# Kernel optimization log

Measured on AMD Instinct MI355X. Metric: run time of the kernel, lower is better.

The kernel has to match this reference:

```python
import jax, jax.numpy as jnp
import numpy as np

N = 50000        # nodes
E = 800000       # edges
G = 256          # graphs in batch
NUM_EMB = 100    # atomic number vocab
D = 64           # atom_emb_dim (node channel dim, constant across layers)
ED = 50          # edge_dim
H = 128          # hidden_dim
L = 4            # num_conv_layers
Z = 2 * D + ED   # CGConv concat dim = 178


def setup_inputs() -> dict:
    key = jax.random.key(0)
    ks = jax.random.split(key, 12)
    x = jax.random.randint(ks[0], (N,), 0, NUM_EMB)
    edge_index = jax.random.randint(ks[1], (2, E), 0, N)
    edge_attr = jax.random.normal(ks[2], (E, ED), dtype=jnp.float32)
    batch = jnp.sort(jax.random.randint(ks[3], (N,), 0, G))
    emb = jax.random.normal(ks[4], (NUM_EMB, D), dtype=jnp.float32) * 0.1
    Wf = jax.random.normal(ks[5], (L, Z, D), dtype=jnp.float32) * (Z ** -0.5)
    bf = jnp.zeros((L, D), jnp.float32)
    Ws = jax.random.normal(ks[6], (L, Z, D), dtype=jnp.float32) * (Z ** -0.5)
    bs = jnp.zeros((L, D), jnp.float32)
    W1 = jax.random.normal(ks[7], (D, H), dtype=jnp.float32) * (D ** -0.5)
    b1 = jnp.zeros((H,), jnp.float32)
    W2 = jax.random.normal(ks[8], (H, H // 2), dtype=jnp.float32) * (H ** -0.5)
    b2 = jnp.zeros((H // 2,), jnp.float32)
    Wo = jax.random.normal(ks[9], (H // 2, 1), dtype=jnp.float32) * ((H // 2) ** -0.5)
    bo = jnp.zeros((1,), jnp.float32)
    return dict(x=x, edge_index=edge_index, edge_attr=edge_attr, batch=batch,
                emb=emb, Wf=Wf, bf=bf, Ws=Ws, bs=bs,
                W1=W1, b1=b1, W2=W2, b2=b2, Wo=Wo, bo=bo)


def reference(x, edge_index, edge_attr, batch, emb, Wf, bf, Ws, bs, W1, b1, W2, b2, Wo, bo):
    src = edge_index[0]  # x_j (source / neighbor)
    dst = edge_index[1]  # x_i (target, aggregation index) -- PyG convention
    h = emb[x]           # [N, D]
    for l in range(L):
        # CGConv message: z = [x_i, x_j, e_ij]; gated message; scatter-add; residual
        z = jnp.concatenate([h[dst], h[src], edge_attr], axis=-1)   # [E, Z]
        msg = jax.nn.sigmoid(z @ Wf[l] + bf[l]) * jax.nn.softplus(z @ Ws[l] + bs[l])  # [E, D]
        agg = jax.ops.segment_sum(msg, dst, num_segments=N)          # [N, D]
        h = jax.nn.softplus(h + agg)                                 # residual + F.softplus
    # global mean pool over graphs
    counts = jax.ops.segment_sum(jnp.ones((N, 1), h.dtype), batch, num_segments=G)
    pooled = jax.ops.segment_sum(h, batch, num_segments=G) / jnp.maximum(counts, 1.0)  # [G, D]
    g = jax.nn.relu(pooled @ W1 + b1)   # dropout is identity in eval mode
    g = jax.nn.relu(g @ W2 + b2)
    return (g @ Wo + bo).reshape(-1)    # [G]
```

## Files before the change

kernel.cpp:

```cpp
#include <hip/hip_runtime.h>
#include <hip/hip_bf16.h>
#include <hip/hip_fp16.h>
#include <math.h>

#define N_NODES 50000
#define N_EDGES 800000
#define N_GRAPHS 256
#define DIM 64
#define EDIM 50
#define HDIM 128
#define NLAYER 4
#define ZDIM (2 * DIM + EDIM)
#define NTILES (N_EDGES / 32)

typedef _Float16 f16;
typedef __attribute__((ext_vector_type(4))) _Float16 half4v;
typedef __attribute__((ext_vector_type(8))) _Float16 half8v;
typedef __attribute__((ext_vector_type(16))) float f32x16;

__device__ __forceinline__ float softplus_f(float x) {
    return fmaxf(x, 0.0f) + log1pf(__expf(-fabsf(x)));
}

__device__ __forceinline__ float sigx(float x) {
    float t = __builtin_amdgcn_exp2f(-1.44269504f * x);
    return __builtin_amdgcn_rcpf(1.0f + t);
}
__device__ __forceinline__ float spx(float y) {
    float t = __builtin_amdgcn_exp2f(-1.44269504f * fabsf(y));
    return fmaxf(y, 0.0f) + 0.69314718f * __builtin_amdgcn_logf(1.0f + t);
}

__global__ void k_wcat(const float* __restrict__ Wf, const float* __restrict__ Ws,
                       f16* __restrict__ wcat) {
    int i = blockIdx.x * 256 + threadIdx.x;
    int l = i >> 13;
    int rem = i & 8191;
    int k = rem >> 7;
    int colv = rem & 127;
    int g = colv >> 6, d = colv & 63;
    float v = 0.0f;
    if (k < 50) {
        const float* W = g ? Ws : Wf;
        v = W[((size_t)l * ZDIM + 128 + k) * 64 + d];
    }
    wcat[i] = (f16)v;
}

__global__ void k_wnode(const float* __restrict__ Wf, const float* __restrict__ Ws,
                        f16* __restrict__ wnode) {
    int i = blockIdx.x * 256 + threadIdx.x;
    int l = i >> 14;
    int rem = i & 16383;
    int colv2 = rem >> 6;
    int k = rem & 63;
    int half = colv2 >> 7, g = (colv2 >> 6) & 1, d = colv2 & 63;
    const float* W = g ? Ws : Wf;
    wnode[i] = (f16)W[((size_t)l * ZDIM + half * 64 + k) * 64 + d];
}

__global__ void k_hist(const int* __restrict__ eidx, int* __restrict__ hist) {
    int e = blockIdx.x * 256 + threadIdx.x;
    atomicAdd(&hist[eidx[N_EDGES + e]], 1);
}

__global__ __launch_bounds__(256) void k_scan1(const int* __restrict__ hist,
                                               int* __restrict__ scanbuf,
                                               int* __restrict__ blocksums) {
    int tid = threadIdx.x;
    int i = blockIdx.x * 256 + tid;
    int v = (i < N_NODES) ? hist[i] : 0;
    int lane = tid & 63;
#pragma unroll
    for (int off = 1; off < 64; off <<= 1) {
        int u = __shfl_up(v, off);
        if (lane >= off) v += u;
    }
    __shared__ int wsum[4];
    if (lane == 63) wsum[tid >> 6] = v;
    __syncthreads();
    int w = tid >> 6;
    int add = 0;
#pragma unroll
    for (int k = 0; k < 3; ++k)
        if (k < w) add += wsum[k];
    v += add;
    if (i < N_NODES) scanbuf[i] = v;
    if (tid == 255) blocksums[blockIdx.x] = v;
}

__global__ __launch_bounds__(256) void k_scan2(int* __restrict__ blocksums, int nb) {
    int tid = threadIdx.x;
    int v = (tid < nb) ? blocksums[tid] : 0;
    int lane = tid & 63;
#pragma unroll
    for (int off = 1; off < 64; off <<= 1) {
        int u = __shfl_up(v, off);
        if (lane >= off) v += u;
    }
    __shared__ int wsum[4];
    if (lane == 63) wsum[tid >> 6] = v;
    __syncthreads();
    int w = tid >> 6;
    int add = 0;
#pragma unroll
    for (int k = 0; k < 3; ++k)
        if (k < w) add += wsum[k];
    v += add;
    if (tid < nb) blocksums[tid] = v;
}

__global__ void k_scan3(const int* __restrict__ scanbuf, const int* __restrict__ hist,
                        const int* __restrict__ blocksums, int* __restrict__ cursor) {
    int i = blockIdx.x * 256 + threadIdx.x;
    if (i >= N_NODES) return;
    int b = blockIdx.x;
    int off = b ? blocksums[b - 1] : 0;
    cursor[i] = scanbuf[i] - hist[i] + off;
}

__global__ void k_scatter(const int* __restrict__ eidx, int* __restrict__ cursor,
                          int* __restrict__ perm, int* __restrict__ permSrc,
                          int* __restrict__ permDst) {
    int e = blockIdx.x * 256 + threadIdx.x;
    int d = eidx[N_EDGES + e];
    int pos = atomicAdd(&cursor[d], 1);
    perm[pos] = e;
    permDst[pos] = d;
    permSrc[pos] = eidx[e];
}

__global__ __launch_bounds__(256) void k_eprep2(const float* __restrict__ eattr,
                                                const int* __restrict__ perm,
                                                f16* __restrict__ eattrP) {
    int i = blockIdx.x * 256 + threadIdx.x;
    int lane = i & 63;
    int tile = i >> 6;
    int pos = tile * 32 + (lane & 31);
    int h2 = lane >> 5;
    int edge = perm[pos];
    const float* erow = eattr + (size_t)edge * EDIM;
    int k0 = 8 * h2;
    float2 v[12];
#pragma unroll
    for (int kk = 0; kk < 3; ++kk) {
#pragma unroll
        for (int p = 0; p < 4; ++p) {
            v[kk * 4 + p] = *(const float2*)(erow + k0 + 16 * kk + 2 * p);
        }
    }
    float2 t48 = make_float2(0.0f, 0.0f);
    if (h2 == 0) t48 = *(const float2*)(erow + 48);

    unsigned fb = ((unsigned)tile * 4u) * 64u + (unsigned)lane;
#pragma unroll
    for (int kk = 0; kk < 3; ++kk) {
        half8v o;
#pragma unroll
        for (int p = 0; p < 4; ++p) {
            o[2 * p] = (f16)v[kk * 4 + p].x;
            o[2 * p + 1] = (f16)v[kk * 4 + p].y;
        }
        *(half8v*)&eattrP[(fb + (unsigned)kk * 64u) * 8u] = o;
    }
    half8v o;
#pragma unroll
    for (int e = 0; e < 8; ++e) o[e] = (f16)0.0f;
    o[0] = (f16)t48.x;
    o[1] = (f16)t48.y;
    *(half8v*)&eattrP[(fb + 192u) * 8u] = o;
}

template <int MODE>
__global__ __launch_bounds__(256) void k_nodemm(
    const float* __restrict__ hin, float* __restrict__ hout, float* __restrict__ agg,
    const int* __restrict__ x, const float* __restrict__ emb,
    const float* __restrict__ bf, const float* __restrict__ bs,
    const f16* __restrict__ wnode_l,
    __half* __restrict__ dstpack, __half* __restrict__ srcpack) {
    __shared__ f16 hsf[64 * 68];
    int tid = threadIdx.x;
    int w = tid >> 6, lane = tid & 63;
    int c = lane & 31, h2 = lane >> 5;
    int n0 = blockIdx.x * 64;
    for (int idx = tid; idx < 64 * 64; idx += 256) {
        int i = idx >> 6, k = idx & 63;
        int n = n0 + i;
        float v = 0.0f;
        if (n < N_NODES) {
            if (MODE == 1) {
                v = softplus_f(hin[(size_t)n * DIM + k] + agg[(size_t)n * DIM + k]);
                agg[(size_t)n * DIM + k] = 0.0f;
                hout[(size_t)n * DIM + k] = v;
            } else {
                v = emb[x[n] * DIM + k];
                hout[(size_t)n * DIM + k] = v;
            }
        }
        hsf[i * 68 + k] = (f16)v;
    }
    __syncthreads();

    half8v bfr[2][4];
#pragma unroll
    for (int nt = 0; nt < 2; ++nt) {
#pragma unroll
        for (int kk = 0; kk < 4; ++kk) {
            bfr[nt][kk] = *(const half8v*)(wnode_l + ((64 * w + 32 * nt + c) * 64 + kk * 16 + 8 * h2));
        }
    }
    float bias[2];
#pragma unroll
    for (int nt = 0; nt < 2; ++nt) {
        int d = 32 * nt + c;
        bias[nt] = (w == 0) ? bf[d] : (w == 1) ? bs[d] : 0.0f;
    }

    f32x16 acc[2][2];
#pragma unroll
    for (int mt = 0; mt < 2; ++mt)
#pragma unroll
        for (int nt = 0; nt < 2; ++nt)
#pragma unroll
            for (int i = 0; i < 16; ++i) acc[mt][nt][i] = 0.0f;

#pragma unroll
    for (int mt = 0; mt < 2; ++mt) {
        half8v afr[4];
#pragma unroll
        for (int kk = 0; kk < 4; ++kk) {
            const f16* ap = &hsf[(32 * mt + c) * 68 + kk * 16 + 8 * h2];
            half8v a;
            *(half4v*)&a = *(const half4v*)ap;
            *((half4v*)&a + 1) = *(const half4v*)(ap + 4);
            afr[kk] = a;
        }
#pragma unroll
        for (int nt = 0; nt < 2; ++nt)
#pragma unroll
            for (int kk = 0; kk < 4; ++kk)
                acc[mt][nt] = __builtin_amdgcn_mfma_f32_32x32x16_f16(afr[kk], bfr[nt][kk],
                                                                     acc[mt][nt], 0, 0, 0);
    }

    __half* outp = (w < 2) ? dstpack : srcpack;
    int colbase = (w & 1) * 64;
#pragma unroll
    for (int mt = 0; mt < 2; ++mt) {
#pragma unroll
        for (int nt = 0; nt < 2; ++nt) {
#pragma unroll
            for (int r = 0; r < 16; ++r) {
                int row = 32 * mt + (r & 3) + 8 * (r >> 2) + 4 * h2;
                int n = n0 + row;
                if (n < N_NODES) {
                    outp[(size_t)n * 128 + colbase + 32 * nt + c] =
                        __float2half(acc[mt][nt][r] + bias[nt]);
                }
            }
        }
    }
}

__global__ __launch_bounds__(256) void k_edge_s(
    const int* __restrict__ permSrc, const int* __restrict__ permDst,
    const f16* __restrict__ eattrP, const __half* __restrict__ dstpack,
    const __half* __restrict__ srcpack, const f16* __restrict__ wcat_l,
    float* __restrict__ agg) {
    __shared__ float msgV[2][64][34];
    __shared__ int dsh[32];
    int tid = threadIdx.x;
    int w = tid >> 6;
    int lane = tid & 63;
    int c = lane & 31;
    int h2 = lane >> 5;
    int col = w * 32 + c;

    half8v wfr[4];
#pragma unroll
    for (int kk = 0; kk < 4; ++kk) {
#pragma unroll
        for (int e = 0; e < 8; ++e) {
            wfr[kk][e] = wcat_l[(kk * 16 + 8 * h2 + e) * 128 + col];
        }
    }

    for (int tile = blockIdx.x; tile < NTILES; tile += gridDim.x) {
        int e0 = tile * 32;
        int tI = permDst[e0 + c];
        int sI = permSrc[e0 + c];
        if (tid < 32) dsh[tid] = tI;

        half8v efr[4];
        unsigned fb = ((unsigned)tile * 4u) * 64u + (unsigned)lane;
#pragma unroll
        for (int kk = 0; kk < 4; ++kk) {
            efr[kk] = *(const half8v*)&eattrP[(fb + (unsigned)kk * 64u) * 8u];
        }

        f32x16 acc;
#pragma unroll
        for (int i = 0; i < 16; ++i) acc[i] = 0.0f;
#pragma unroll
        for (int kk = 0; kk < 4; ++kk) {
            acc = __builtin_amdgcn_mfma_f32_32x32x16_f16(wfr[kk], efr[kk], acc, 0, 0, 0);
        }

        const __half* drow = dstpack + (((size_t)(unsigned)tI) << 7) + w * 32 + 4 * h2;
        const __half* srow = srcpack + (((size_t)(unsigned)sI) << 7) + w * 32 + 4 * h2;
        float dv[4][4], sv[4][4];
#pragma unroll
        for (int q = 0; q < 4; ++q) {
            const __half2* dp = (const __half2*)(drow + 8 * q);
            float2 lo = __half22float2(dp[0]);
            float2 hi = __half22float2(dp[1]);
            dv[q][0] = lo.x; dv[q][1] = lo.y; dv[q][2] = hi.x; dv[q][3] = hi.y;
        }
#pragma unroll
        for (int q = 0; q < 4; ++q) {
            const __half2* sp = (const __half2*)(srow + 8 * q);
            float2 lo = __half22float2(sp[0]);
            float2 hi = __half22float2(sp[1]);
            sv[q][0] = lo.x; sv[q][1] = lo.y; sv[q][2] = hi.x; sv[q][3] = hi.y;
        }

        int dbase = (w & 1) * 32 + 4 * h2;
        if (w < 2) {
#pragma unroll
            for (int q = 0; q < 4; ++q) {
#pragma unroll
                for (int i = 0; i < 4; ++i) {
                    float pre = acc[4 * q + i] + dv[q][i] + sv[q][i];
                    msgV[0][dbase + 8 * q + i][c] = sigx(pre);
                }
            }
        } else {
#pragma unroll
            for (int q = 0; q < 4; ++q) {
#pragma unroll
                for (int i = 0; i < 4; ++i) {
                    float pre = acc[4 * q + i] + dv[q][i] + sv[q][i];
                    msgV[1][dbase + 8 * q + i][c] = spx(pre);
                }
            }
        }

        __syncthreads();

        {
            int d = tid & 63;
            int base = (tid >> 6) * 8;
            float m[8];
#pragma unroll
            for (int j2 = 0; j2 < 4; ++j2) {
                float2 a = *(const float2*)&msgV[0][d][base + 2 * j2];
                float2 b = *(const float2*)&msgV[1][d][base + 2 * j2];
                m[2 * j2] = a.x * b.x;
                m[2 * j2 + 1] = a.y * b.y;
            }
            float accum = 0.0f;
            int cur = dsh[base];
#pragma unroll
            for (int j = 0; j < 8; ++j) {
                int dn = dsh[base + j];
                if (dn != cur) {
                    unsafeAtomicAdd(&agg[(unsigned)((cur << 6) + d)], accum);
                    accum = 0.0f;
                    cur = dn;
                }
                accum += m[j];
            }
            unsafeAtomicAdd(&agg[(unsigned)((cur << 6) + d)], accum);
        }
        __syncthreads();
    }
}

__global__ __launch_bounds__(256) void k_edge_u(
    const int* __restrict__ eidx, const float* __restrict__ eattr,
    const __half* __restrict__ dstpack, const __half* __restrict__ srcpack,
    const f16* __restrict__ wcat_l, float* __restrict__ agg) {
    __shared__ float msgV[2][32][64];
    __shared__ int dsh[32], ssh[32];
    int tid = threadIdx.x;
    int w = tid >> 6;
    int lane = tid & 63;
    int c = lane & 31;
    int h2 = lane >> 5;
    int col = w * 32 + c;
    int dcol = (w & 1) * 32 + c;

    half8v bfr[4];
#pragma unroll
    for (int kk = 0; kk < 4; ++kk) {
#pragma unroll
        for (int e = 0; e < 8; ++e) bfr[kk][e] = wcat_l[(kk * 16 + 8 * h2 + e) * 128 + col];
    }

    for (int tile = blockIdx.x; tile < NTILES; tile += gridDim.x) {
        int e0 = tile * 32;
        if (lane < 32) {
            dsh[lane] = eidx[N_EDGES + e0 + lane];
            ssh[lane] = eidx[e0 + lane];
        }
        half8v afr[4];
        const float* erow = eattr + (size_t)(e0 + c) * EDIM;
#pragma unroll
        for (int kk = 0; kk < 3; ++kk) {
            int k0 = kk * 16 + 8 * h2;
#pragma unroll
            for (int p = 0; p < 4; ++p) {
                float2 v = *(const float2*)(erow + k0 + 2 * p);
                afr[kk][2 * p] = (f16)v.x;
                afr[kk][2 * p + 1] = (f16)v.y;
            }
        }
        {
            half8v a;
#pragma unroll
            for (int e = 0; e < 8; ++e) a[e] = (f16)0.0f;
            if (h2 == 0) {
                float2 v = *(const float2*)(erow + 48);
                a[0] = (f16)v.x;
                a[1] = (f16)v.y;
            }
            afr[3] = a;
        }
        f32x16 acc;
#pragma unroll
        for (int i = 0; i < 16; ++i) acc[i] = 0.0f;
#pragma unroll
        for (int kk = 0; kk < 4; ++kk)
            acc = __builtin_amdgcn_mfma_f32_32x32x16_f16(afr[kk], bfr[kk], acc, 0, 0, 0);

        __builtin_amdgcn_wave_barrier();

#pragma unroll
        for (int grp = 0; grp < 2; ++grp) {
            int tI[8], sI[8];
            float dv[8], sv[8];
#pragma unroll
            for (int r = 0; r < 8; ++r) {
                int rr = grp * 8 + r;
                int row = (rr & 3) + 8 * (rr >> 2) + 4 * h2;
                tI[r] = dsh[row];
                sI[r] = ssh[row];
            }
#pragma unroll
            for (int r = 0; r < 8; ++r) {
                dv[r] = __half2float(dstpack[(unsigned)((tI[r] << 7) + col)]);
                sv[r] = __half2float(srcpack[(unsigned)((sI[r] << 7) + col)]);
            }
            float pre[8];
#pragma unroll
            for (int r = 0; r < 8; ++r) pre[r] = acc[grp * 8 + r] + dv[r] + sv[r];
            if (w < 2) {
#pragma unroll
                for (int r = 0; r < 8; ++r) {
                    int rr = grp * 8 + r;
                    int row = (rr & 3) + 8 * (rr >> 2) + 4 * h2;
                    msgV[0][row][dcol] = sigx(pre[r]);
                }
            } else {
#pragma unroll
                for (int r = 0; r < 8; ++r) {
                    int rr = grp * 8 + r;
                    int row = (rr & 3) + 8 * (rr >> 2) + 4 * h2;
                    msgV[1][row][dcol] = spx(pre[r]);
                }
            }
        }
        __syncthreads();
        {
            int d = tid & 63;
            int base = (tid >> 6) * 8;
#pragma unroll
            for (int j = 0; j < 8; ++j) {
                int row = base + j;
                float m = msgV[0][row][d] * msgV[1][row][d];
                unsafeAtomicAdd(&agg[(unsigned)((dsh[row] << 6) + d)], m);
            }
        }
        __syncthreads();
    }
}

__global__ __launch_bounds__(256) void k_pool_s(
    const float* __restrict__ h, const float* __restrict__ agg,
    const int* __restrict__ batch,
    float* __restrict__ pooled, float* __restrict__ counts) {
    int tid = threadIdx.x;
    int d = tid & 63;
    int strm = tid >> 6;
    int base = blockIdx.x * 256 + strm * 64;
    if (base >= N_NODES) return;
    int end = min(base + 64, N_NODES);
    float accum = 0.0f;
    int cnt = 0;
    int cur = batch[base];
    for (int n = base; n < end; ++n) {
        int g = batch[n];
        if (g != cur) {
            unsafeAtomicAdd(&pooled[cur * DIM + d], accum);
            if (d == 0) unsafeAtomicAdd(&counts[cur], (float)cnt);
            accum = 0.0f;
            cnt = 0;
            cur = g;
        }
        accum += softplus_f(h[(size_t)n * DIM + d] + agg[(size_t)n * DIM + d]);
        cnt++;
    }
    unsafeAtomicAdd(&pooled[cur * DIM + d], accum);
    if (d == 0) unsafeAtomicAdd(&counts[cur], (float)cnt);
}

__global__ __launch_bounds__(64) void k_mlp(
    const float* __restrict__ pooled, const float* __restrict__ counts,
    const float* __restrict__ W1, const float* __restrict__ b1,
    const float* __restrict__ W2, const float* __restrict__ b2,
    const float* __restrict__ Wo, const float* __restrict__ bo,
    float* __restrict__ out) {
    __shared__ float ps[64];
    __shared__ float h1[128];
    int g = blockIdx.x, lane = threadIdx.x;
    float cnt = fmaxf(counts[g], 1.0f);
    ps[lane] = pooled[g * DIM + lane] / cnt;
    __syncthreads();
#pragma unroll
    for (int rep = 0; rep < 2; ++rep) {
        int j = lane + rep * 64;
        float acc = b1[j];
        for (int k = 0; k < 64; ++k) acc += ps[k] * W1[k * HDIM + j];
        h1[j] = fmaxf(acc, 0.0f);
    }
    __syncthreads();
    float acc = b2[lane];
    for (int k = 0; k < 128; ++k) acc += h1[k] * W2[k * 64 + lane];
    float v = fmaxf(acc, 0.0f) * Wo[lane];
#pragma unroll
    for (int off = 32; off; off >>= 1) v += __shfl_down(v, off);
    if (lane == 0) out[g] = v + bo[0];
}

extern "C" void kernel_launch(void* const* d_in, const int* in_sizes, int n_in,
                              void* d_out, int out_size, void* d_ws, size_t ws_size,
                              hipStream_t stream) {
    const int* x = (const int*)d_in[0];
    const int* eidx = (const int*)d_in[1];
    const float* eattr = (const float*)d_in[2];
    const int* batch = (const int*)d_in[3];
    const float* emb = (const float*)d_in[4];
    const float* Wf = (const float*)d_in[5];
    const float* bf = (const float*)d_in[6];
    const float* Ws = (const float*)d_in[7];
    const float* bs = (const float*)d_in[8];
    const float* W1 = (const float*)d_in[9];
    const float* b1 = (const float*)d_in[10];
    const float* W2 = (const float*)d_in[11];
    const float* b2 = (const float*)d_in[12];
    const float* Wo = (const float*)d_in[13];
    const float* bo = (const float*)d_in[14];
    float* out = (float*)d_out;

    char* p = (char*)d_ws;
    float* h = (float*)p;        p += (size_t)N_NODES * DIM * 4;
    __half* dstpack = (__half*)p; p += (size_t)N_NODES * 2 * DIM * 2;
    __half* srcpack = (__half*)p; p += (size_t)N_NODES * 2 * DIM * 2;
    float* agg = (float*)p;      p += (size_t)N_NODES * DIM * 4;
    float* pooled = (float*)p;   p += (size_t)N_GRAPHS * DIM * 4;
    float* counts = (float*)p;   p += (size_t)N_GRAPHS * 4;
    f16* wcat = (f16*)p;         p += (size_t)NLAYER * 64 * 128 * 2;
    f16* wnode = (f16*)p;        p += (size_t)NLAYER * 256 * 64 * 2;
    f16* eattrP = (f16*)p;       p += (size_t)NTILES * 4 * 64 * 8 * 2;
    int* hist = (int*)p;         p += (size_t)N_NODES * 4;
    int* scanbuf = (int*)p;      p += (size_t)N_NODES * 4;
    int* blocksums = (int*)p;    p += 256 * 4;
    int* cursor = (int*)p;       p += (size_t)N_NODES * 4;
    int* perm = (int*)p;         p += (size_t)N_EDGES * 4;
    int* permSrc = (int*)p;      p += (size_t)N_EDGES * 4;
    int* permDst = (int*)p;      p += (size_t)N_EDGES * 4;
    size_t used_sorted = (size_t)(p - (char*)d_ws);

    bool sorted = used_sorted <= ws_size;

    const int SCAN_BLOCKS = (N_NODES + 255) / 256;
    const int NODEMM_BLOCKS = (N_NODES + 63) / 64;

    k_wcat<<<NLAYER * 64 * 128 / 256, 256, 0, stream>>>(Wf, Ws, wcat);
    k_wnode<<<NLAYER * 256 * 64 / 256, 256, 0, stream>>>(Wf, Ws, wnode);
    if (sorted) {
        hipMemsetAsync(hist, 0, (size_t)N_NODES * 4, stream);
        k_hist<<<N_EDGES / 256, 256, 0, stream>>>(eidx, hist);
        k_scan1<<<SCAN_BLOCKS, 256, 0, stream>>>(hist, scanbuf, blocksums);
        k_scan2<<<1, 256, 0, stream>>>(blocksums, SCAN_BLOCKS);
        k_scan3<<<SCAN_BLOCKS, 256, 0, stream>>>(scanbuf, hist, blocksums, cursor);
        k_scatter<<<N_EDGES / 256, 256, 0, stream>>>(eidx, cursor, perm, permSrc, permDst);
        k_eprep2<<<NTILES * 64 / 256, 256, 0, stream>>>(eattr, perm, eattrP);
    }
    hipMemsetAsync(agg, 0,
                   (size_t)N_NODES * DIM * 4 + (size_t)N_GRAPHS * DIM * 4 + N_GRAPHS * 4,
                   stream);
    for (int l = 0; l < NLAYER; ++l) {
        const f16* wnl = wnode + (size_t)l * 256 * 64;
        if (l == 0) {
            k_nodemm<2><<<NODEMM_BLOCKS, 256, 0, stream>>>(
                nullptr, h, nullptr, x, emb, bf + l * DIM, bs + l * DIM, wnl,
                dstpack, srcpack);
        } else {
            k_nodemm<1><<<NODEMM_BLOCKS, 256, 0, stream>>>(
                h, h, agg, nullptr, nullptr, bf + l * DIM, bs + l * DIM, wnl,
                dstpack, srcpack);
        }
        if (sorted) {
            k_edge_s<<<2048, 256, 0, stream>>>(permSrc, permDst, eattrP, dstpack, srcpack,
                                               wcat + (size_t)l * 64 * 128, agg);
        } else {
            k_edge_u<<<2048, 256, 0, stream>>>(eidx, eattr, dstpack, srcpack,
                                               wcat + (size_t)l * 64 * 128, agg);
        }
    }
    k_pool_s<<<(N_NODES + 255) / 256, 256, 0, stream>>>(h, agg, batch, pooled, counts);
    k_mlp<<<N_GRAPHS, 64, 0, stream>>>(pooled, counts, W1, b1, W2, b2, Wo, bo, out);
}
```

Baseline: 678.9 us.

## Prefetch next edge tile in sorted edge kernel, lighter LDS barriers, merge weight prep

The persistent sorted-edge kernel now loads the next tile's dst/src indices and packed edge attributes into registers while it processes the current tile. This hides global load latency behind the MFMA and atomic work. __syncthreads is replaced with a barrier that waits only on LDS counters, so outstanding global loads no longer stall at each barrier. The two weight-prep kernels are merged into one launch. The cost is extra register pressure from the prefetch buffers.

```diff
diff --git a/kernel.cpp b/kernel.cpp
--- a/kernel.cpp
+++ b/kernel.cpp
@@ -31,32 +31,38 @@
     return fmaxf(y, 0.0f) + 0.69314718f * __builtin_amdgcn_logf(1.0f + t);
 }
 
-__global__ void k_wcat(const float* __restrict__ Wf, const float* __restrict__ Ws,
-                       f16* __restrict__ wcat) {
+__device__ __forceinline__ void lds_barrier() {
+    __builtin_amdgcn_sched_barrier(0);
+    asm volatile("s_waitcnt lgkmcnt(0)" ::: "memory");
+    __builtin_amdgcn_s_barrier();
+    __builtin_amdgcn_sched_barrier(0);
+}
+
+__global__ void k_wprep(const float* __restrict__ Wf, const float* __restrict__ Ws,
+                        f16* __restrict__ wcat, f16* __restrict__ wnode) {
     int i = blockIdx.x * 256 + threadIdx.x;
-    int l = i >> 13;
-    int rem = i & 8191;
-    int k = rem >> 7;
-    int colv = rem & 127;
-    int g = colv >> 6, d = colv & 63;
-    float v = 0.0f;
-    if (k < 50) {
+    if (i < 32768) {
+        int l = i >> 13;
+        int rem = i & 8191;
+        int k = rem >> 7;
+        int colv = rem & 127;
+        int g = colv >> 6, d = colv & 63;
+        float v = 0.0f;
+        if (k < 50) {
+            const float* W = g ? Ws : Wf;
+            v = W[((size_t)l * ZDIM + 128 + k) * 64 + d];
+        }
+        wcat[i] = (f16)v;
+    } else {
+        int j = i - 32768;
+        int l = j >> 14;
+        int rem = j & 16383;
+        int colv2 = rem >> 6;
+        int k = rem & 63;
+        int half = colv2 >> 7, g = (colv2 >> 6) & 1, d = colv2 & 63;
         const float* W = g ? Ws : Wf;
-        v = W[((size_t)l * ZDIM + 128 + k) * 64 + d];
-    }
-    wcat[i] = (f16)v;
-}
-
-__global__ void k_wnode(const float* __restrict__ Wf, const float* __restrict__ Ws,
-                        f16* __restrict__ wnode) {
-    int i = blockIdx.x * 256 + threadIdx.x;
-    int l = i >> 14;
-    int rem = i & 16383;
-    int colv2 = rem >> 6;
-    int k = rem & 63;
-    int half = colv2 >> 7, g = (colv2 >> 6) & 1, d = colv2 & 63;
-    const float* W = g ? Ws : Wf;
-    wnode[i] = (f16)W[((size_t)l * ZDIM + half * 64 + k) * 64 + d];
+        wnode[j] = (f16)W[((size_t)l * ZDIM + half * 64 + k) * 64 + d];
+    }
 }
 
 __global__ void k_hist(const int* __restrict__ eidx, int* __restrict__ hist) {
@@ -285,17 +291,34 @@
         }
     }
 
-    for (int tile = blockIdx.x; tile < NTILES; tile += gridDim.x) {
-        int e0 = tile * 32;
-        int tI = permDst[e0 + c];
-        int sI = permSrc[e0 + c];
+    int tile = blockIdx.x;
+    int tI = permDst[tile * 32 + c];
+    int sI = permSrc[tile * 32 + c];
+    half8v efr[4];
+    {
+        unsigned fb = ((unsigned)tile * 4u) * 64u + (unsigned)lane;
+#pragma unroll
+        for (int kk = 0; kk < 4; ++kk)
+            efr[kk] = *(const half8v*)&eattrP[(fb + (unsigned)kk * 64u) * 8u];
+    }
+
+    while (true) {
         if (tid < 32) dsh[tid] = tI;
 
-        half8v efr[4];
-        unsigned fb = ((unsigned)tile * 4u) * 64u + (unsigned)lane;
-#pragma unroll
-        for (int kk = 0; kk < 4; ++kk) {
-            efr[kk] = *(const half8v*)&eattrP[(fb + (unsigned)kk * 64u) * 8u];
+        int nt = tile + gridDim.x;
+        bool havenext = nt < NTILES;
+        int tIn = tI, sIn = sI;
+        half8v efn[4];
+        if (havenext) {
+            tIn = permDst[nt * 32 + c];
+            sIn = permSrc[nt * 32 + c];
+            unsigned fbn = ((unsigned)nt * 4u) * 64u + (unsigned)lane;
+#pragma unroll
+            for (int kk = 0; kk < 4; ++kk)
+                efn[kk] = *(const half8v*)&eattrP[(fbn + (unsigned)kk * 64u) * 8u];
+        } else {
+#pragma unroll
+            for (int kk = 0; kk < 4; ++kk) efn[kk] = efr[kk];
         }
 
         f32x16 acc;
@@ -345,7 +368,7 @@
             }
         }
 
-        __syncthreads();
+        lds_barrier();
 
         {
             int d = tid & 63;
@@ -372,7 +395,15 @@
             }
             unsafeAtomicAdd(&agg[(unsigned)((cur << 6) + d)], accum);
         }
-        __syncthreads();
+
+        lds_barrier();
+
+        if (!havenext) break;
+        tile = nt;
+        tI = tIn;
+        sI = sIn;
+#pragma unroll
+        for (int kk = 0; kk < 4; ++kk) efr[kk] = efn[kk];
     }
 }
 
@@ -586,8 +617,7 @@
     const int SCAN_BLOCKS = (N_NODES + 255) / 256;
     const int NODEMM_BLOCKS = (N_NODES + 63) / 64;
 
-    k_wcat<<<NLAYER * 64 * 128 / 256, 256, 0, stream>>>(Wf, Ws, wcat);
-    k_wnode<<<NLAYER * 256 * 64 / 256, 256, 0, stream>>>(Wf, Ws, wnode);
+    k_wprep<<<(32768 + 65536) / 256, 256, 0, stream>>>(Wf, Ws, wcat, wnode);
     if (sorted) {
         hipMemsetAsync(hist, 0, (size_t)N_NODES * 4, stream);
         k_hist<<<N_EDGES / 256, 256, 0, stream>>>(eidx, hist);
```

Measured after the change: 697.8 us. 2.8% more time.
